# Kernel optimization log

Measured on AMD Instinct MI355X. Metric: run time of the kernel, lower is better.

The kernel has to match this reference:

```python
import jax, jax.numpy as jnp
import numpy as np

B, S, H = 32, 2048, 1024
A = 1024  # attention_hidden_size
EPS = 1e-5


def setup_inputs() -> dict:
    key = jax.random.key(0)
    ks = jax.random.split(key, 16)
    sc_h = 1.0 / np.sqrt(H)
    sc_a = 1.0 / np.sqrt(A)
    sc_2h = 1.0 / np.sqrt(2 * H)
    return {
        "seq_states": jax.random.normal(ks[0], (B, S, H), jnp.float32),
        "q_state": jax.random.normal(ks[1], (B, H), jnp.float32),
        "Wk": jax.random.uniform(ks[2], (H, A), jnp.float32, -sc_h, sc_h),
        "bk": jax.random.uniform(ks[3], (A,), jnp.float32, -sc_h, sc_h),
        "Wq": jax.random.uniform(ks[4], (H, A), jnp.float32, -sc_h, sc_h),
        "bq": jax.random.uniform(ks[5], (A,), jnp.float32, -sc_h, sc_h),
        "Wg": jax.random.uniform(ks[6], (A, A), jnp.float32, -sc_a, sc_a),
        "bg": jax.random.uniform(ks[7], (A,), jnp.float32, -sc_a, sc_a),
        "Ws": jax.random.uniform(ks[8], (A, 1), jnp.float32, -sc_a, sc_a),
        "bs": jax.random.uniform(ks[9], (1,), jnp.float32, -sc_a, sc_a),
        "Wo": jax.random.uniform(ks[10], (2 * H, H), jnp.float32, -sc_2h, sc_2h),
        "bo": jax.random.uniform(ks[11], (H,), jnp.float32, -sc_2h, sc_2h),
        "gamma": jnp.ones((H,), jnp.float32),
        "beta": jnp.zeros((H,), jnp.float32),
    }


def reference(seq_states, q_state, Wk, bk, Wq, bq, Wg, bg, Ws, bs, Wo, bo, gamma, beta):
    keys = jnp.einsum("bsh,ha->bsa", seq_states, Wk) + bk          # [B,S,A]
    query = (q_state @ Wq + bq)[:, None, :]                          # [B,1,A]
    alignment = jnp.tanh(keys + query)                               # [B,S,A]
    gate = jax.nn.sigmoid(jnp.einsum("bsa,ac->bsc", alignment, Wg) + bg)
    gated = alignment * gate                                         # dropout p=0.0 -> identity
    scores = jnp.einsum("bsa,ao->bso", gated, Ws)[..., 0] + bs[0]    # [B,S]
    weights = jax.nn.softmax(scores, axis=1)                         # [B,S]
    context = jnp.einsum("bs,bsh->bh", weights, seq_states)          # [B,H]
    fused_in = jnp.concatenate([context, q_state], axis=-1)          # [B,2H]
    pre = fused_in @ Wo + bo + q_state                               # residual
    mu = jnp.mean(pre, axis=-1, keepdims=True)
    var = jnp.var(pre, axis=-1, keepdims=True)
    fused = (pre - mu) * jax.lax.rsqrt(var + EPS) * gamma + beta
    return (fused, weights)
```

## Files before the change

### kernel.cpp

```cpp
#include <hip/hip_runtime.h>

typedef __attribute__((ext_vector_type(8))) short bf16x8;
typedef __attribute__((ext_vector_type(8))) unsigned short ushort8;
typedef __attribute__((ext_vector_type(4))) unsigned short ushortx4;
typedef __attribute__((ext_vector_type(4))) float f32x4;

__device__ __forceinline__ unsigned short f2bf(float f) {
  union { float f; unsigned u; } c; c.f = f;
  return (unsigned short)((c.u + 0x7fffu + ((c.u >> 16) & 1u)) >> 16);
}
__device__ __forceinline__ float bf2f(unsigned short u) {
  union { unsigned u; float f; } c; c.u = ((unsigned)u) << 16;
  return c.f;
}
__device__ __forceinline__ float fast_tanh(float x) {
  float e = __expf(2.f * x);
  return 1.f - 2.f * __builtin_amdgcn_rcpf(e + 1.f);
}
__device__ __forceinline__ float fast_sigmoid(float x) {
  return __builtin_amdgcn_rcpf(1.f + __expf(-x));
}
__device__ __forceinline__ void gload16(const void* g, void* lds) {
  __builtin_amdgcn_global_load_lds(
      (const __attribute__((address_space(1))) unsigned int*)g,
      (__attribute__((address_space(3))) unsigned int*)lds, 16, 0, 0);
}
__device__ __forceinline__ void bar() {
  asm volatile("" ::: "memory");
  __builtin_amdgcn_s_barrier();
  asm volatile("" ::: "memory");
}
__device__ __forceinline__ void vwait0() {
  asm volatile("s_waitcnt vmcnt(0)" ::: "memory");
}

__device__ __forceinline__ void mfma16_4(const bf16x8 (&a)[4], const bf16x8 (&b)[4],
                                         f32x4 (&acc)[4][4]) {
#pragma unroll
  for (int i = 0; i < 4; ++i)
#pragma unroll
    for (int n = 0; n < 4; ++n)
      acc[i][n] =
          __builtin_amdgcn_mfma_f32_16x16x32_bf16(a[i], b[n], acc[i][n], 0, 0, 0);
}

#define GEMM128_SETUP(Ag, Bg)                                                            \
  int lin = (blockIdx.x & 7) * 512 + (blockIdx.x >> 3);                                  \
  int mt = lin >> 3, nt = lin & 7;                                                       \
  int m0 = mt * 128, n0 = nt * 128;                                                      \
  int t = threadIdx.x, lane = t & 63, wave = t >> 6;                                     \
  int wr = wave >> 1, wc = wave & 1;                                                     \
  int sl0 = ((lane >> 4) ^ (lane & 7)) * 16;                                             \
  int sl1 = (((lane >> 4) + 4) ^ (lane & 7)) * 16;                                       \
  const char* rAk0 = (const char*)As + (wr * 64 + (lane & 15)) * 128 + sl0;              \
  const char* rAk1 = (const char*)As + (wr * 64 + (lane & 15)) * 128 + sl1;              \
  const char* rBk0 = (const char*)Bs + (wc * 64 + (lane & 15)) * 128 + sl0;              \
  const char* rBk1 = (const char*)Bs + (wc * 64 + (lane & 15)) * 128 + sl1;              \
  int l3 = t >> 3;                                                                       \
  int sgE = ((t & 7) ^ (l3 & 7)) * 8;                                                    \
  const unsigned short* pA = Ag + (size_t)(m0 + l3) * 1024 + sgE;                        \
  const unsigned short* pB = Bg + (size_t)(n0 + l3) * 1024 + sgE;                        \
  char* dA = (char*)As + t * 16;                                                         \
  char* dB = (char*)Bs + t * 16;                                                         \
  f32x4 acc[4][4] = {};                                                                  \
  _Pragma("unroll 1") for (int kt = 0; kt < 16; ++kt) {                                  \
    int k0 = kt * 64;                                                                    \
    _Pragma("unroll") for (int r = 0; r < 4; ++r) {                                      \
      gload16(pA + (size_t)(r * 32) * 1024 + k0, dA + r * 4096);                         \
      gload16(pB + (size_t)(r * 32) * 1024 + k0, dB + r * 4096);                         \
    }                                                                                    \
    vwait0();                                                                            \
    bar();                                                                               \
    {                                                                                    \
      bf16x8 a[4], b[4];                                                                 \
      _Pragma("unroll") for (int i = 0; i < 4; ++i)                                      \
          a[i] = *(const bf16x8*)(rAk0 + i * 2048);                                      \
      _Pragma("unroll") for (int n = 0; n < 4; ++n)                                      \
          b[n] = *(const bf16x8*)(rBk0 + n * 2048);                                      \
      mfma16_4(a, b, acc);                                                               \
      _Pragma("unroll") for (int i = 0; i < 4; ++i)                                      \
          a[i] = *(const bf16x8*)(rAk1 + i * 2048);                                      \
      _Pragma("unroll") for (int n = 0; n < 4; ++n)                                      \
          b[n] = *(const bf16x8*)(rBk1 + n * 2048);                                      \
      mfma16_4(a, b, acc);                                                               \
    }                                                                                    \
    bar();                                                                               \
  }

__global__ __launch_bounds__(256) void prep_kernel(
    const float* __restrict__ seq, unsigned short* __restrict__ seqb,
    const float* __restrict__ Wk, const float* __restrict__ Wg,
    unsigned short* __restrict__ WkT, unsigned short* __restrict__ WgT,
    const float* __restrict__ q, const float* __restrict__ Wq,
    float* __restrict__ qp) {
  __shared__ float smem[4160];
  int bid = blockIdx.x, t = threadIdx.x;
  if (bid < 2048) {
    size_t i = ((size_t)bid * 256 + t) * 8;
    const size_t stride = (size_t)2048 * 256 * 8;
    for (; i < (size_t)67108864; i += stride) {
      f32x4 v0 = *(const f32x4*)(seq + i);
      f32x4 v1 = *(const f32x4*)(seq + i + 4);
      ushort8 o;
#pragma unroll
      for (int k = 0; k < 4; ++k) { o[k] = f2bf(v0[k]); o[k + 4] = f2bf(v1[k]); }
      *(ushort8*)(seqb + i) = o;
    }
  } else if (bid < 2560) {
    int b2 = bid - 2048;
    int mat = b2 >> 8;
    int tid = b2 & 255;
    int tr = tid >> 4, tc = tid & 15;
    const float* src = mat ? Wg : Wk;
    unsigned short* dst = mat ? WgT : WkT;
    int r0 = tr * 64, c0 = tc * 64;
    int lr = t >> 6, lc = t & 63;
#pragma unroll
    for (int i = 0; i < 16; ++i) {
      int r = i * 4 + lr;
      smem[r * 65 + lc] = src[(size_t)(r0 + r) * 1024 + c0 + lc];
    }
    __syncthreads();
#pragma unroll
    for (int i = 0; i < 16; ++i) {
      int r = i * 4 + lr;
      dst[(size_t)(c0 + r) * 1024 + r0 + lc] = f2bf(smem[lc * 65 + r]);
    }
  } else {
    int b3 = bid - 2560;
    int ac = b3 & 3, hc = b3 >> 2;
    int h0 = hc * 128;
    for (int i = t; i < 4096; i += 256) {
      int b = i >> 7, hh = i & 127;
      smem[b * 128 + hh] = q[(size_t)b * 1024 + h0 + hh];
    }
    __syncthreads();
    int a = ac * 256 + t;
    float acc[32] = {};
    for (int hh = 0; hh < 128; hh += 4) {
      float w0 = Wq[(size_t)(h0 + hh) * 1024 + a];
      float w1 = Wq[(size_t)(h0 + hh + 1) * 1024 + a];
      float w2 = Wq[(size_t)(h0 + hh + 2) * 1024 + a];
      float w3 = Wq[(size_t)(h0 + hh + 3) * 1024 + a];
#pragma unroll
      for (int b = 0; b < 32; ++b) {
        f32x4 qv = *(const f32x4*)&smem[b * 128 + hh];
        acc[b] += qv[0] * w0 + qv[1] * w1 + qv[2] * w2 + qv[3] * w3;
      }
    }
#pragma unroll
    for (int b = 0; b < 32; ++b) qp[((size_t)(hc * 32 + b)) * 1024 + a] = acc[b];
  }
}

__global__ __launch_bounds__(256, 2) void gemm1_kernel(
    const unsigned short* __restrict__ seqb, const unsigned short* __restrict__ WkT,
    const float* __restrict__ qp, const float* __restrict__ bq,
    const float* __restrict__ bk, unsigned short* __restrict__ alignb) {
  __shared__ unsigned short As[128 * 64];
  __shared__ unsigned short Bs[128 * 64];
  GEMM128_SETUP(seqb, WkT)

  int bidx = m0 >> 11;
  float qv[4];
#pragma unroll
  for (int ni = 0; ni < 4; ++ni) {
    int col = n0 + wc * 64 + ni * 16 + (lane & 15);
    float s = bq[col] + bk[col];
#pragma unroll
    for (int hc = 0; hc < 8; ++hc) s += qp[((size_t)(hc * 32 + bidx)) * 1024 + col];
    qv[ni] = s;
  }
#pragma unroll
  for (int mi = 0; mi < 4; ++mi) {
    int row0 = m0 + wr * 64 + mi * 16 + ((lane >> 4) * 4);
#pragma unroll
    for (int ni = 0; ni < 4; ++ni) {
      int col = n0 + wc * 64 + ni * 16 + (lane & 15);
#pragma unroll
      for (int j = 0; j < 4; ++j) {
        float v = fast_tanh(acc[mi][ni][j] + qv[ni]);
        alignb[(size_t)(row0 + j) * 1024 + col] = f2bf(v);
      }
    }
  }
}

__global__ __launch_bounds__(256, 2) void gemm2_kernel(
    const unsigned short* __restrict__ alignb, const unsigned short* __restrict__ WgT,
    const float* __restrict__ bg, const float* __restrict__ Ws,
    float* __restrict__ scores_part) {
  __shared__ unsigned short As[128 * 64];
  __shared__ unsigned short Bs[128 * 64];
  __shared__ float sred[128 * 2];
  GEMM128_SETUP(alignb, WgT)

#pragma unroll
  for (int mi = 0; mi < 4; ++mi) {
#pragma unroll
    for (int j = 0; j < 4; ++j) {
      int rloc = wr * 64 + mi * 16 + ((lane >> 4) * 4) + j;
      int row = m0 + rloc;
      float p = 0.f;
#pragma unroll
      for (int ni = 0; ni < 4; ++ni) {
        int col = n0 + wc * 64 + ni * 16 + (lane & 15);
        float gate = fast_sigmoid(acc[mi][ni][j] + bg[col]);
        float al = bf2f(alignb[(size_t)row * 1024 + col]);
        p += al * gate * Ws[col];
      }
      p += __shfl_xor(p, 1);
      p += __shfl_xor(p, 2);
      p += __shfl_xor(p, 4);
      p += __shfl_xor(p, 8);
      if ((lane & 15) == 0) sred[rloc * 2 + wc] = p;
    }
  }
  __syncthreads();
  if (t < 128) scores_part[(size_t)nt * 65536 + m0 + t] = sred[t * 2] + sred[t * 2 + 1];
}

__global__ __launch_bounds__(256) void softmax_kernel(const float* __restrict__ sp,
                                                      float* __restrict__ wout) {
  __shared__ float red[256];
  int b = blockIdx.x, t = threadIdx.x;
  float sc[8];
  float lmax = -1e30f;
#pragma unroll
  for (int i = 0; i < 8; ++i) {
    int s = i * 256 + t;
    float v = 0.f;
#pragma unroll
    for (int n = 0; n < 8; ++n) v += sp[(size_t)n * 65536 + b * 2048 + s];
    sc[i] = v;
    lmax = fmaxf(lmax, v);
  }
  red[t] = lmax;
  __syncthreads();
  for (int off = 128; off > 0; off >>= 1) {
    if (t < off) red[t] = fmaxf(red[t], red[t + off]);
    __syncthreads();
  }
  float mx = red[0];
  __syncthreads();
  float lsum = 0.f;
#pragma unroll
  for (int i = 0; i < 8; ++i) {
    sc[i] = expf(sc[i] - mx);
    lsum += sc[i];
  }
  red[t] = lsum;
  __syncthreads();
  for (int off = 128; off > 0; off >>= 1) {
    if (t < off) red[t] += red[t + off];
    __syncthreads();
  }
  float inv = 1.f / red[0];
#pragma unroll
  for (int i = 0; i < 8; ++i) wout[(size_t)b * 2048 + i * 256 + t] = sc[i] * inv;
}

__global__ __launch_bounds__(256) void context_kernel(const unsigned short* __restrict__ seqb,
                                                      const float* __restrict__ wts,
                                                      float* __restrict__ ctx_part) {
  __shared__ float wsh[128];
  int b = blockIdx.x, t = threadIdx.x, s0 = blockIdx.z * 128;
  int h0 = t * 4;
  if (t < 128) wsh[t] = wts[(size_t)b * 2048 + s0 + t];
  __syncthreads();
  float a0 = 0.f, a1 = 0.f, a2 = 0.f, a3 = 0.f;
  const unsigned short* p = seqb + ((size_t)b * 2048 + s0) * 1024 + h0;
#pragma unroll 4
  for (int s = 0; s < 128; ++s) {
    ushortx4 v = *(const ushortx4*)(p + (size_t)s * 1024);
    float w = wsh[s];
    a0 += w * bf2f(v[0]);
    a1 += w * bf2f(v[1]);
    a2 += w * bf2f(v[2]);
    a3 += w * bf2f(v[3]);
  }
  float* dst = ctx_part + (size_t)(blockIdx.z * 32 + b) * 1024 + h0;
  dst[0] = a0; dst[1] = a1; dst[2] = a2; dst[3] = a3;
}

__global__ __launch_bounds__(256) void pre_kernel(const float* __restrict__ ctx_part,
                                                  const float* __restrict__ q,
                                                  const float* __restrict__ Wo,
                                                  float* __restrict__ pre_part) {
  __shared__ float fin[32 * 128];
  int kc = blockIdx.x, hc = blockIdx.y, t = threadIdx.x;
  int k0 = kc * 128, h0 = hc * 256;
  for (int i = t; i < 4096; i += 256) {
    int b = i >> 7, kk = i & 127, k = k0 + kk;
    float f;
    if (k < 1024) {
      f = 0.f;
#pragma unroll
      for (int s = 0; s < 16; ++s) f += ctx_part[((size_t)(s * 32 + b)) * 1024 + k];
    } else {
      f = q[(size_t)b * 1024 + (k - 1024)];
    }
    fin[b * 128 + kk] = f;
  }
  __syncthreads();
  int h = h0 + t;
  float acc[32] = {};
  for (int kk = 0; kk < 128; kk += 4) {
    float w0 = Wo[(size_t)(k0 + kk) * 1024 + h];
    float w1 = Wo[(size_t)(k0 + kk + 1) * 1024 + h];
    float w2 = Wo[(size_t)(k0 + kk + 2) * 1024 + h];
    float w3 = Wo[(size_t)(k0 + kk + 3) * 1024 + h];
#pragma unroll
    for (int b = 0; b < 32; ++b) {
      f32x4 fv = *(const f32x4*)&fin[b * 128 + kk];
      acc[b] += fv[0] * w0 + fv[1] * w1 + fv[2] * w2 + fv[3] * w3;
    }
  }
#pragma unroll
  for (int b = 0; b < 32; ++b) pre_part[((size_t)(kc * 32 + b)) * 1024 + h] = acc[b];
}

__global__ __launch_bounds__(256) void ln_kernel(const float* __restrict__ pre_part,
                                                 const float* __restrict__ q,
                                                 const float* __restrict__ bo,
                                                 const float* __restrict__ gamma,
                                                 const float* __restrict__ beta,
                                                 float* __restrict__ outF) {
  __shared__ float red[256];
  int b = blockIdx.x, t = threadIdx.x;
  float v[4];
  float lsum = 0.f;
#pragma unroll
  for (int i = 0; i < 4; ++i) {
    int h = i * 256 + t;
    float x = bo[h] + q[(size_t)b * 1024 + h];
#pragma unroll
    for (int kc = 0; kc < 16; ++kc) x += pre_part[((size_t)(kc * 32 + b)) * 1024 + h];
    v[i] = x;
    lsum += x;
  }
  red[t] = lsum;
  __syncthreads();
  for (int off = 128; off > 0; off >>= 1) {
    if (t < off) red[t] += red[t + off];
    __syncthreads();
  }
  float mu = red[0] * (1.f / 1024.f);
  __syncthreads();
  float lv = 0.f;
#pragma unroll
  for (int i = 0; i < 4; ++i) {
    float d = v[i] - mu;
    lv += d * d;
  }
  red[t] = lv;
  __syncthreads();
  for (int off = 128; off > 0; off >>= 1) {
    if (t < off) red[t] += red[t + off];
    __syncthreads();
  }
  float var = red[0] * (1.f / 1024.f);
  float rs = rsqrtf(var + 1e-5f);
#pragma unroll
  for (int i = 0; i < 4; ++i) {
    int h = i * 256 + t;
    outF[(size_t)b * 1024 + h] = (v[i] - mu) * rs * gamma[h] + beta[h];
  }
}

extern "C" void kernel_launch(void* const* d_in, const int* in_sizes, int n_in,
                              void* d_out, int out_size, void* d_ws, size_t ws_size,
                              hipStream_t stream) {
  const float* seq = (const float*)d_in[0];
  const float* q = (const float*)d_in[1];
  const float* Wk = (const float*)d_in[2];
  const float* bk = (const float*)d_in[3];
  const float* Wq = (const float*)d_in[4];
  const float* bq = (const float*)d_in[5];
  const float* Wg = (const float*)d_in[6];
  const float* bg = (const float*)d_in[7];
  const float* Ws = (const float*)d_in[8];
  const float* Wo = (const float*)d_in[10];
  const float* bo = (const float*)d_in[11];
  const float* gamma = (const float*)d_in[12];
  const float* beta = (const float*)d_in[13];

  float* outF = (float*)d_out;
  float* outW = outF + 32 * 1024;

  char* ws = (char*)d_ws;
  unsigned short* alignb = (unsigned short*)ws;  ws += (size_t)134217728;
  unsigned short* seqb = (unsigned short*)ws;    ws += (size_t)134217728;
  unsigned short* WkT = (unsigned short*)ws;     ws += 2097152;
  unsigned short* WgT = (unsigned short*)ws;     ws += 2097152;
  float* qp = (float*)ws;                        ws += 1048576;
  float* scores_part = (float*)ws;               ws += 2097152;
  float* ctx_part = (float*)ws;                  ws += 2097152;
  float* pre_part = (float*)ws;                  ws += 2097152;
  if (ws_size < (size_t)(ws - (char*)d_ws)) return;

  prep_kernel<<<2592, 256, 0, stream>>>(seq, seqb, Wk, Wg, WkT, WgT, q, Wq, qp);
  gemm1_kernel<<<4096, 256, 0, stream>>>(seqb, WkT, qp, bq, bk, alignb);
  gemm2_kernel<<<4096, 256, 0, stream>>>(alignb, WgT, bg, Ws, scores_part);
  softmax_kernel<<<32, 256, 0, stream>>>(scores_part, outW);
  context_kernel<<<dim3(32, 1, 16), 256, 0, stream>>>(seqb, outW, ctx_part);
  pre_kernel<<<dim3(16, 4), 256, 0, stream>>>(ctx_part, q, Wo, pre_part);
  ln_kernel<<<32, 256, 0, stream>>>(pre_part, q, bo, gamma, beta, outF);
}
```

Measured before the change: 483.3 us.

## Fuse seq fp32-to-bf16 conversion into gemm1 tile loads and drop seqb buffer

Removes the standalone pass that converted the full seq_states tensor to bf16. That pass read the whole fp32 tensor and wrote a bf16 copy, which is a large amount of HBM traffic. gemm1 now loads fp32 A tiles straight into a larger LDS buffer with global_load_lds and converts them to bf16 in registers right before the MFMAs. context_kernel now reads fp32 seq directly. The trade-offs are twice the A-tile bytes per gemm1 block, more LDS per block, and double the read traffic in context_kernel, in exchange for eliminating the conversion pass and its workspace buffer.

Result: slower. 495.4 us (+2.5%).

```diff
diff --git a/kernel.cpp b/kernel.cpp
--- a/kernel.cpp
+++ b/kernel.cpp
@@ -1,4 +1,5 @@
 #include <hip/hip_runtime.h>
+#include <hip/hip_bf16.h>
 
 typedef __attribute__((ext_vector_type(8))) short bf16x8;
 typedef __attribute__((ext_vector_type(8))) unsigned short ushort8;
@@ -32,6 +33,15 @@
 }
 __device__ __forceinline__ void vwait0() {
   asm volatile("s_waitcnt vmcnt(0)" ::: "memory");
+}
+__device__ __forceinline__ bf16x8 cvt8(f32x4 v0, f32x4 v1) {
+  union { bf16x8 v; unsigned short h[8]; } o;
+#pragma unroll
+  for (int k = 0; k < 4; ++k) {
+    o.h[k] = __hip_bfloat16_raw(__float2bfloat16(v0[k])).x;
+    o.h[k + 4] = __hip_bfloat16_raw(__float2bfloat16(v1[k])).x;
+  }
+  return o.v;
 }
 
 __device__ __forceinline__ void mfma16_4(const bf16x8 (&a)[4], const bf16x8 (&b)[4],
@@ -88,28 +98,15 @@
   }
 
 __global__ __launch_bounds__(256) void prep_kernel(
-    const float* __restrict__ seq, unsigned short* __restrict__ seqb,
     const float* __restrict__ Wk, const float* __restrict__ Wg,
     unsigned short* __restrict__ WkT, unsigned short* __restrict__ WgT,
     const float* __restrict__ q, const float* __restrict__ Wq,
     float* __restrict__ qp) {
   __shared__ float smem[4160];
   int bid = blockIdx.x, t = threadIdx.x;
-  if (bid < 2048) {
-    size_t i = ((size_t)bid * 256 + t) * 8;
-    const size_t stride = (size_t)2048 * 256 * 8;
-    for (; i < (size_t)67108864; i += stride) {
-      f32x4 v0 = *(const f32x4*)(seq + i);
-      f32x4 v1 = *(const f32x4*)(seq + i + 4);
-      ushort8 o;
-#pragma unroll
-      for (int k = 0; k < 4; ++k) { o[k] = f2bf(v0[k]); o[k + 4] = f2bf(v1[k]); }
-      *(ushort8*)(seqb + i) = o;
-    }
-  } else if (bid < 2560) {
-    int b2 = bid - 2048;
-    int mat = b2 >> 8;
-    int tid = b2 & 255;
+  if (bid < 512) {
+    int mat = bid >> 8;
+    int tid = bid & 255;
     int tr = tid >> 4, tc = tid & 15;
     const float* src = mat ? Wg : Wk;
     unsigned short* dst = mat ? WgT : WkT;
@@ -127,7 +124,7 @@
       dst[(size_t)(c0 + r) * 1024 + r0 + lc] = f2bf(smem[lc * 65 + r]);
     }
   } else {
-    int b3 = bid - 2560;
+    int b3 = bid - 512;
     int ac = b3 & 3, hc = b3 >> 2;
     int h0 = hc * 128;
     for (int i = t; i < 4096; i += 256) {
@@ -154,18 +151,68 @@
 }
 
 __global__ __launch_bounds__(256, 2) void gemm1_kernel(
-    const unsigned short* __restrict__ seqb, const unsigned short* __restrict__ WkT,
+    const float* __restrict__ seq, const unsigned short* __restrict__ WkT,
     const float* __restrict__ qp, const float* __restrict__ bq,
     const float* __restrict__ bk, unsigned short* __restrict__ alignb) {
-  __shared__ unsigned short As[128 * 64];
+  __shared__ float As[128 * 64];
   __shared__ unsigned short Bs[128 * 64];
-  GEMM128_SETUP(seqb, WkT)
+  int lin = (blockIdx.x & 7) * 512 + (blockIdx.x >> 3);
+  int mt = lin >> 3, nt = lin & 7;
+  int m0 = mt * 128, n0 = nt * 128;
+  int t = threadIdx.x, lane = t & 63, wave = t >> 6;
+  int wr = wave >> 1, wc = wave & 1;
+  int l15 = lane & 15, g = lane >> 4;
+  int sl0 = (g ^ (lane & 7)) * 16;
+  int sl1 = ((g + 4) ^ (lane & 7)) * 16;
+  const char* rBk0 = (const char*)Bs + (wc * 64 + l15) * 128 + sl0;
+  const char* rBk1 = (const char*)Bs + (wc * 64 + l15) * 128 + sl1;
+  const char* aRow = (const char*)As + (wr * 64 + l15) * 256;
+  const char* rA00 = aRow + (((2 * g) ^ l15) * 16);
+  const char* rA01 = aRow + ((((2 * g) | 1) ^ l15) * 16);
+  const char* rA10 = aRow + ((((2 * g) ^ 8) ^ l15) * 16);
+  const char* rA11 = aRow + (((((2 * g) | 1) ^ 8) ^ l15) * 16);
+  int sgA = ((t & 15) ^ (t >> 4)) * 4;
+  const float* pAf = seq + (size_t)(m0 + (t >> 4)) * 1024 + sgA;
+  int l3 = t >> 3;
+  int sgE = ((t & 7) ^ (l3 & 7)) * 8;
+  const unsigned short* pB = WkT + (size_t)(n0 + l3) * 1024 + sgE;
+  char* dA = (char*)As + t * 16;
+  char* dB = (char*)Bs + t * 16;
+  f32x4 acc[4][4] = {};
+#pragma unroll 1
+  for (int kt = 0; kt < 16; ++kt) {
+    int k0 = kt * 64;
+#pragma unroll
+    for (int r = 0; r < 8; ++r)
+      gload16(pAf + (size_t)(r * 16) * 1024 + k0, dA + r * 4096);
+#pragma unroll
+    for (int r = 0; r < 4; ++r)
+      gload16(pB + (size_t)(r * 32) * 1024 + k0, dB + r * 4096);
+    vwait0();
+    bar();
+    {
+      bf16x8 a[4], b[4];
+#pragma unroll
+      for (int i = 0; i < 4; ++i)
+        a[i] = cvt8(*(const f32x4*)(rA00 + i * 4096), *(const f32x4*)(rA01 + i * 4096));
+#pragma unroll
+      for (int n = 0; n < 4; ++n) b[n] = *(const bf16x8*)(rBk0 + n * 2048);
+      mfma16_4(a, b, acc);
+#pragma unroll
+      for (int i = 0; i < 4; ++i)
+        a[i] = cvt8(*(const f32x4*)(rA10 + i * 4096), *(const f32x4*)(rA11 + i * 4096));
+#pragma unroll
+      for (int n = 0; n < 4; ++n) b[n] = *(const bf16x8*)(rBk1 + n * 2048);
+      mfma16_4(a, b, acc);
+    }
+    bar();
+  }
 
   int bidx = m0 >> 11;
   float qv[4];
 #pragma unroll
   for (int ni = 0; ni < 4; ++ni) {
-    int col = n0 + wc * 64 + ni * 16 + (lane & 15);
+    int col = n0 + wc * 64 + ni * 16 + l15;
     float s = bq[col] + bk[col];
 #pragma unroll
     for (int hc = 0; hc < 8; ++hc) s += qp[((size_t)(hc * 32 + bidx)) * 1024 + col];
@@ -176,7 +223,7 @@
     int row0 = m0 + wr * 64 + mi * 16 + ((lane >> 4) * 4);
 #pragma unroll
     for (int ni = 0; ni < 4; ++ni) {
-      int col = n0 + wc * 64 + ni * 16 + (lane & 15);
+      int col = n0 + wc * 64 + ni * 16 + l15;
 #pragma unroll
       for (int j = 0; j < 4; ++j) {
         float v = fast_tanh(acc[mi][ni][j] + qv[ni]);
@@ -260,7 +307,7 @@
   for (int i = 0; i < 8; ++i) wout[(size_t)b * 2048 + i * 256 + t] = sc[i] * inv;
 }
 
-__global__ __launch_bounds__(256) void context_kernel(const unsigned short* __restrict__ seqb,
+__global__ __launch_bounds__(256) void context_kernel(const float* __restrict__ seq,
                                                       const float* __restrict__ wts,
                                                       float* __restrict__ ctx_part) {
   __shared__ float wsh[128];
@@ -269,15 +316,15 @@
   if (t < 128) wsh[t] = wts[(size_t)b * 2048 + s0 + t];
   __syncthreads();
   float a0 = 0.f, a1 = 0.f, a2 = 0.f, a3 = 0.f;
-  const unsigned short* p = seqb + ((size_t)b * 2048 + s0) * 1024 + h0;
+  const float* p = seq + ((size_t)b * 2048 + s0) * 1024 + h0;
 #pragma unroll 4
   for (int s = 0; s < 128; ++s) {
-    ushortx4 v = *(const ushortx4*)(p + (size_t)s * 1024);
+    f32x4 v = *(const f32x4*)(p + (size_t)s * 1024);
     float w = wsh[s];
-    a0 += w * bf2f(v[0]);
-    a1 += w * bf2f(v[1]);
-    a2 += w * bf2f(v[2]);
-    a3 += w * bf2f(v[3]);
+    a0 += w * v[0];
+    a1 += w * v[1];
+    a2 += w * v[2];
+    a3 += w * v[3];
   }
   float* dst = ctx_part + (size_t)(blockIdx.z * 32 + b) * 1024 + h0;
   dst[0] = a0; dst[1] = a1; dst[2] = a2; dst[3] = a3;
@@ -390,7 +437,6 @@
 
   char* ws = (char*)d_ws;
   unsigned short* alignb = (unsigned short*)ws;  ws += (size_t)134217728;
-  unsigned short* seqb = (unsigned short*)ws;    ws += (size_t)134217728;
   unsigned short* WkT = (unsigned short*)ws;     ws += 2097152;
   unsigned short* WgT = (unsigned short*)ws;     ws += 2097152;
   float* qp = (float*)ws;                        ws += 1048576;
@@ -399,11 +445,11 @@
   float* pre_part = (float*)ws;                  ws += 2097152;
   if (ws_size < (size_t)(ws - (char*)d_ws)) return;
 
-  prep_kernel<<<2592, 256, 0, stream>>>(seq, seqb, Wk, Wg, WkT, WgT, q, Wq, qp);
-  gemm1_kernel<<<4096, 256, 0, stream>>>(seqb, WkT, qp, bq, bk, alignb);
+  prep_kernel<<<544, 256, 0, stream>>>(Wk, Wg, WkT, WgT, q, Wq, qp);
+  gemm1_kernel<<<4096, 256, 0, stream>>>(seq, WkT, qp, bq, bk, alignb);
   gemm2_kernel<<<4096, 256, 0, stream>>>(alignb, WgT, bg, Ws, scores_part);
   softmax_kernel<<<32, 256, 0, stream>>>(scores_part, outW);
-  context_kernel<<<dim3(32, 1, 16), 256, 0, stream>>>(seqb, outW, ctx_part);
+  context_kernel<<<dim3(32, 1, 16), 256, 0, stream>>>(seq, outW, ctx_part);
   pre_kernel<<<dim3(16, 4), 256, 0, stream>>>(ctx_part, q, Wo, pre_part);
   ln_kernel<<<32, 256, 0, stream>>>(pre_part, q, bo, gamma, beta, outF);
 }
```
